# Kernel optimization log

Hardware: AMD Instinct MI355X
Metric: run time of the kernel (lower is better)

Reference implementation:

```python
import jax, jax.numpy as jnp
import numpy as np

NEARZERO = 1e-5
# Parameter bounds in dict order: BETA, FC, K0, K1, K2, LP, PERC, UZL, TT, CFMAX, CFR, CWH
BOUNDS = np.array([[1.0, 6.0], [50.0, 1000.0], [0.05, 0.9], [0.01, 0.5],
                   [0.001, 0.2], [0.2, 1.0], [0.0, 10.0], [0.0, 100.0],
                   [-2.5, 2.5], [0.5, 10.0], [0.0, 0.1], [0.0, 0.2]],
                  dtype=np.float32)


def setup_inputs() -> dict:
    key = jax.random.key(0)
    k1, k2, k3, k4 = jax.random.split(key, 4)
    T, G, nmul = 730, 4000, 8
    prcp = jax.random.uniform(k1, (T, G), dtype=jnp.float32) * 10.0   # mm/day, >= 0
    tmean = jax.random.normal(k2, (T, G), dtype=jnp.float32) * 10.0   # deg C
    pet = jax.random.uniform(k3, (T, G), dtype=jnp.float32) * 5.0     # mm/day, >= 0
    x_hydro_model = jnp.stack([prcp, tmean, pet], axis=-1)            # [T, G, 3]
    params_raw = jax.random.uniform(k4, (1, G, 12, nmul), dtype=jnp.float32)  # in [0,1)
    return {"x_hydro_model": x_hydro_model, "params_raw": params_raw}


def _hbv_forward(x_hydro_model, params_raw):
    G = x_hydro_model.shape[1]
    nmul = params_raw.shape[-1]
    b = jnp.asarray(BOUNDS)
    # change_param_range: param * (ub - lb) + lb, static slice at static_idx=-1
    p = params_raw[-1] * (b[:, 1] - b[:, 0])[None, :, None] + b[:, 0][None, :, None]  # [G,12,nmul]
    (BETA, FC, K0, K1, K2, LP, PERCc, UZL, TT, CFMAX, CFR, CWH) = [p[:, i, :] for i in range(12)]

    Pm = x_hydro_model[:, :, 0][:, :, None]    # [T, G, 1] broadcasts over nmul
    Tm = x_hydro_model[:, :, 1][:, :, None]
    PETm = x_hydro_model[:, :, 2][:, :, None]

    init = jnp.full((G, nmul), 0.001, dtype=jnp.float32)
    carry0 = (init, init, init, init, init)  # SNOWPACK, MELTWATER, SM, SUZ, SLZ

    def step(carry, inputs):
        SNOWPACK, MELTWATER, SM, SUZ, SLZ = carry
        PRECIP, Tt, PETt = inputs  # each [G, 1]
        is_rain = (Tt >= TT).astype(jnp.float32)
        RAIN = PRECIP * is_rain
        SNOW = PRECIP * (1.0 - is_rain)
        SNOWPACK = SNOWPACK + SNOW
        melt = jnp.minimum(jnp.maximum(CFMAX * (Tt - TT), 0.0), SNOWPACK)
        MELTWATER = MELTWATER + melt
        SNOWPACK = SNOWPACK - melt
        refreezing = jnp.minimum(jnp.maximum(CFR * CFMAX * (TT - Tt), 0.0), MELTWATER)
        SNOWPACK = SNOWPACK + refreezing
        MELTWATER = MELTWATER - refreezing
        tosoil = jnp.maximum(MELTWATER - CWH * SNOWPACK, 0.0)
        MELTWATER = MELTWATER - tosoil
        soil_wetness = jnp.clip((SM / FC) ** BETA, 0.0, 1.0)
        recharge = (RAIN + tosoil) * soil_wetness
        SM = SM + RAIN + tosoil - recharge
        excess = jnp.maximum(SM - FC, 0.0)
        SM = SM - excess
        evapfactor = jnp.clip(SM / (LP * FC), 0.0, 1.0)
        ETact = jnp.minimum(SM, PETt * evapfactor)
        SM = jnp.maximum(SM - ETact, NEARZERO)
        SUZ = SUZ + recharge + excess
        PERC = jnp.minimum(SUZ, PERCc)
        SUZ = SUZ - PERC
        Q0 = K0 * jnp.maximum(SUZ - UZL, 0.0)
        SUZ = SUZ - Q0
        Q1 = K1 * SUZ
        SUZ = SUZ - Q1
        SLZ = SLZ + PERC
        Q2 = K2 * SLZ
        SLZ = SLZ - Q2
        return (SNOWPACK, MELTWATER, SM, SUZ, SLZ), Q0 + Q1 + Q2

    _, Qsimmu = jax.lax.scan(step, carry0, (Pm, Tm, PETm))  # [T, G, nmul]
    return Qsimmu


def reference(x_hydro_model, params_raw):
    return _hbv_forward(x_hydro_model, params_raw)
```

## Files before the change

### kernel.cpp

```cpp
#include <hip/hip_runtime.h>
#include <math.h>
#include <stdint.h>

#define NM 8
#define NPAR 12
#define KS 32
#define NLL 3

typedef __attribute__((address_space(1))) const void gv_t;
typedef __attribute__((address_space(3))) void lv_t;
typedef float v2f __attribute__((ext_vector_type(2)));

__global__ __launch_bounds__(128, 1) void hbv_kernel(
    const float* __restrict__ x,
    const float* __restrict__ praw,
    float* __restrict__ out,
    int G, int T)
{
    __shared__ float  fbuf[2][(KS + 2) * 24];
    __shared__ float2 ring[2][KS + 2][64];

    const int wid  = threadIdx.x >> 6;
    const int lane = threadIdx.x & 63;
    const int b    = blockIdx.x;
    const int g0   = b << 3;
    const int gl   = lane >> 3;
    const int m    = lane & 7;
    const int g    = g0 + gl;

    const float lb[NPAR] = {1.0f, 50.0f, 0.05f, 0.01f, 0.001f, 0.2f, 0.0f, 0.0f, -2.5f, 0.5f, 0.0f, 0.0f};
    const float ub[NPAR] = {6.0f, 1000.0f, 0.9f, 0.5f, 0.2f, 1.0f, 10.0f, 100.0f, 2.5f, 10.0f, 0.1f, 0.2f};

    float p[NPAR];
    const float* pr = praw + (size_t)g * (NPAR * NM) + m;
    #pragma unroll
    for (int i = 0; i < NPAR; ++i) p[i] = pr[i * NM] * (ub[i] - lb[i]) + lb[i];

    const int NBLK = (T + KS - 1) / KS;

    #define ISSUE_F(fa_, pt_, e_)                                              \
        asm volatile("ds_read2_b32 %0, %2 offset0:0 offset1:1\n\t"             \
                     "ds_read_b32 %1, %2 offset:8"                             \
                     : "=v"(pt_), "=v"(e_) : "v"(fa_));
    #define WAIT_F(pt_, e_, P_, T_, E_)                                        \
        asm volatile("s_waitcnt lgkmcnt(2)\n\t"                                \
                     "v_mov_b32 %0, %3\n\t"                                    \
                     "v_mov_b32 %1, %4\n\t"                                    \
                     "v_mov_b32 %2, %5"                                        \
                     : "=v"(P_), "=v"(T_), "=v"(E_)                            \
                     : "v"(pt_.x), "v"(pt_.y), "v"(e_));
    #define ISSUE_C(ca_, rel_)                                                 \
        asm volatile("ds_read_b64 %0, %1" : "=v"(rel_) : "v"(ca_));
    #define WAIT_C(rel_, rt_, E_)                                              \
        asm volatile("s_waitcnt lgkmcnt(1)\n\t"                                \
                     "v_mov_b32 %0, %2\n\t"                                    \
                     "v_mov_b32 %1, %3"                                        \
                     : "=v"(rt_), "=v"(E_) : "v"(rel_.x), "v"(rel_.y));

    if (wid == 0) {
        const float TT = p[8], CFMAX = p[9], CFR = p[10], CWH = p[11];
        const float nCFMAX_TT   = -(CFMAX * TT);
        const float nCFRCFMAX   = -(CFR * CFMAX);
        const float CFRCFMAX_TT = (CFR * CFMAX) * TT;

        float SP = 0.001f, MW = 0.001f;

        const char* xb = (const char*)x;
        const uint32_t xstep  = (uint32_t)G * 12u;
        const uint32_t gbase  = (uint32_t)g0 * 12u;
        const uint32_t lin    = (uint32_t)lane * 16u;
        const uint32_t r0     = lin / 96u;
        const uint32_t c0     = lin % 96u;
        const uint32_t rowmax = (uint32_t)(T - 1);

        #define ISSUE_CHUNK(cs_, nb_)                                          \
        {                                                                      \
            uint32_t row_ = (uint32_t)(cs_) + r0;                              \
            uint32_t col_ = c0;                                                \
            _Pragma("unroll")                                                  \
            for (int i_ = 0; i_ < NLL; ++i_) {                                 \
                const uint32_t rg_ = row_ < rowmax ? row_ : rowmax;            \
                const uint32_t go_ = rg_ * xstep + gbase + col_;               \
                __builtin_amdgcn_global_load_lds((gv_t*)(xb + go_),            \
                    (lv_t*)&fbuf[nb_][i_ * 256], 16, 0, 0);                    \
                         \
                row_ += 10u + (col_ >= 32u ? 1u : 0u);                         \
                col_  = (col_ >= 32u) ? (col_ - 32u) : (col_ + 64u);           \
            }                                                                  \
        }

        ISSUE_CHUNK(0, 0)

        for (int r = 0; r <= NBLK; ++r) {
            if (r < NBLK) {
                if (r + 1 < NBLK) {
                    ISSUE_CHUNK((r + 1) * KS, (r + 1) & 1)
                    asm volatile("s_waitcnt vmcnt(3)" ::: "memory");
                } else {
                    asm volatile("s_waitcnt vmcnt(0)" ::: "memory");
                }
                const int cnt = (T - r * KS < KS) ? (T - r * KS) : KS;
                uint32_t fa = (uint32_t)(uintptr_t)&fbuf[r & 1][gl * 3];
                float2*  R  = &ring[r & 1][0][lane];

                v2f pt0, pt1; float e0, e1;
                ISSUE_F(fa, pt0, e0) fa += 96;
                ISSUE_F(fa, pt1, e1) fa += 96;

                #define PROD_STEP(PT_, E_)                                     \
                {                                                              \
                    float P, Tt, E;                                            \
                    WAIT_F(PT_, E_, P, Tt, E)                                  \
                    ISSUE_F(fa, PT_, E_) fa += 96;    \
                    const float RAIN = (Tt >= TT) ? P : 0.0f;                  \
                    const float SNOW = P - RAIN;                               \
                    const float mc = fmaxf(fmaf(CFMAX, Tt, nCFMAX_TT), 0.0f);  \
                    const float rc = fmaxf(fmaf(nCFRCFMAX, Tt, CFRCFMAX_TT), 0.0f); \
                    SP += SNOW;                                                \
                    const float melt = fminf(mc, SP);                          \
                    MW += melt;                                                \
                    SP -= melt;                                                \
                    const float refr = fminf(rc, MW);                          \
                    SP += refr;                                                \
                    MW -= refr;                                                \
                    const float cw = CWH * SP;                                 \
                    const float ts = fmaxf(MW - cw, 0.0f);                     \
                    MW = fminf(MW, cw);                                        \
                    float2 rel; rel.x = RAIN + ts; rel.y = E;                  \
                    *R = rel;                                                  \
                    R += 64;                                                   \
                }

                for (int tt = 0; tt < cnt; tt += 2) {
                    PROD_STEP(pt0, e0)
                    PROD_STEP(pt1, e1)
                }
                #undef PROD_STEP
            }
            __syncthreads();
        }
        #undef ISSUE_CHUNK
    } else {
        const float BETA = p[0], FC = p[1], K0 = p[2], K1 = p[3], K2 = p[4],
                    LP = p[5], PERCc = p[6], UZL = p[7];
        const float invLPFC = 1.0f / (LP * FC);
        const float nBLFC   = -BETA * __builtin_amdgcn_logf(FC);
        const float OMK0    = 1.0f - K0;
        const float K0UZL   = K0 * UZL;
        const float OMK1    = 1.0f - K1;
        const float OMK2    = 1.0f - K2;

        float SM = 0.001f, SUZ = 0.001f, SLZ = 0.001f;

        char* ob = (char*)out;
        uint32_t ooff = (uint32_t)(g * NM + m) * 4u;
        const uint32_t ostep = (uint32_t)(G * NM) * 4u;

        for (int r = 0; r <= NBLK; ++r) {
            if (r >= 1) {
                const int base = (r - 1) * KS;
                const int cnt  = (T - base < KS) ? (T - base) : KS;
                uint32_t ca = (uint32_t)(uintptr_t)&ring[(r - 1) & 1][0][lane];

                v2f rel0, rel1;
                ISSUE_C(ca, rel0) ca += 512;
                ISSUE_C(ca, rel1) ca += 512;

                #define CONS_STEP(REL_)                                        \
                {                                                              \
                    float rt, E;                                               \
                    WAIT_C(REL_, rt, E)                                        \
                    ISSUE_C(ca, REL_) ca += 512;      \
                    const float lg = __builtin_amdgcn_logf(SM);                \
                    const float bl = fminf(fmaf(BETA, lg, nBLFC), 0.0f);       \
                    const float sw = __builtin_amdgcn_exp2f(bl);               \
                    const float rg = rt * sw;                                  \
                    const float SM1 = SM + rt - rg;                            \
                    const float ex = fmaxf(SM1 - FC, 0.0f);                    \
                    const float SM2 = fminf(SM1, FC);                          \
                    const float omPe = fmaf(-E, invLPFC, 1.0f);                \
                    SM = fmaxf(fmaxf(SM2 * omPe, SM2 - E), 1e-5f);   \
                    SUZ = SUZ + rg + ex;                                       \
                    const float pc = fminf(SUZ, PERCc);                        \
                    const float s2 = fmaxf(SUZ - PERCc, 0.0f);                 \
                    const float s3 = fminf(s2, fmaf(OMK0, s2, K0UZL));         \
                    const float s4 = s3 * OMK1;                                \
                    SUZ = s4;                                                  \
                    const float sl = SLZ + pc;                                 \
                    const float q2 = K2 * sl;                                  \
                    SLZ = sl * OMK2;                                           \
                    const float Q = (s2 - s4) + q2;                            \
                    *(float*)(ob + ooff) = Q;                                  \
                    ooff += ostep;                                             \
                }

                for (int tt = 0; tt < cnt; tt += 2) {
                    CONS_STEP(rel0)
                    CONS_STEP(rel1)
                }
                #undef CONS_STEP
            }
            __syncthreads();
        }
    }
    #undef ISSUE_F
    #undef WAIT_F
    #undef ISSUE_C
    #undef WAIT_C
}

extern "C" void kernel_launch(void* const* d_in, const int* in_sizes, int n_in,
                              void* d_out, int out_size, void* d_ws, size_t ws_size,
                              hipStream_t stream) {
    const float* x    = (const float*)d_in[0];
    const float* praw = (const float*)d_in[1];
    float* out = (float*)d_out;

    const int G = in_sizes[1] / (NPAR * NM);
    const int T = in_sizes[0] / (3 * G);

    const int grid = G / 8;
    hbv_kernel<<<grid, 128, 0, stream>>>(x, praw, out, G, T);
}
```

Measured before the change: 70.88 us.

## Process two nmul members per lane and 16 gauges per block

Each lane now advances two independent HBV state chains (two nmul members) instead of one, so one block covers 16 gauges and the grid is halved. The forcing tile row width and the ring entries grow to 128-bit writes and reads, and outputs are stored as float2. The time chunk size drops from 32 to 16. The aim is to add instruction-level parallelism to the serial recurrence and to amortise LDS traffic, at the cost of half as many blocks (250 for G=4000), which lowers occupancy across the CUs.

Result: slower. 104.8 us (+47.8%).

```diff
diff --git a/kernel.cpp b/kernel.cpp
--- a/kernel.cpp
+++ b/kernel.cpp
@@ -4,12 +4,15 @@
 
 #define NM 8
 #define NPAR 12
-#define KS 32
+#define GPB 16
+#define KS 16
+#define ROWDW (GPB*3)
 #define NLL 3
 
 typedef __attribute__((address_space(1))) const void gv_t;
 typedef __attribute__((address_space(3))) void lv_t;
 typedef float v2f __attribute__((ext_vector_type(2)));
+typedef float v4f __attribute__((ext_vector_type(4)));
 
 __global__ __launch_bounds__(128, 1) void hbv_kernel(
     const float* __restrict__ x,
@@ -17,24 +20,27 @@
     float* __restrict__ out,
     int G, int T)
 {
-    __shared__ float  fbuf[2][(KS + 2) * 24];
-    __shared__ float2 ring[2][KS + 2][64];
+    __shared__ float fbuf[2][(KS + 2) * ROWDW];
+    __shared__ v4f   ring[2][KS + 2][64];
 
     const int wid  = threadIdx.x >> 6;
     const int lane = threadIdx.x & 63;
     const int b    = blockIdx.x;
-    const int g0   = b << 3;
-    const int gl   = lane >> 3;
-    const int m    = lane & 7;
-    const int g    = g0 + gl;
+    const int gl   = lane >> 2;
+    const int m0   = (lane & 3) << 1;
+    const int g    = (b << 4) + gl;
 
     const float lb[NPAR] = {1.0f, 50.0f, 0.05f, 0.01f, 0.001f, 0.2f, 0.0f, 0.0f, -2.5f, 0.5f, 0.0f, 0.0f};
     const float ub[NPAR] = {6.0f, 1000.0f, 0.9f, 0.5f, 0.2f, 1.0f, 10.0f, 100.0f, 2.5f, 10.0f, 0.1f, 0.2f};
 
-    float p[NPAR];
-    const float* pr = praw + (size_t)g * (NPAR * NM) + m;
+    float pA[NPAR], pB[NPAR];
+    const float* pr = praw + (size_t)g * (NPAR * NM) + m0;
     #pragma unroll
-    for (int i = 0; i < NPAR; ++i) p[i] = pr[i * NM] * (ub[i] - lb[i]) + lb[i];
+    for (int i = 0; i < NPAR; ++i) {
+        const float s = ub[i] - lb[i];
+        pA[i] = pr[i * NM]     * s + lb[i];
+        pB[i] = pr[i * NM + 1] * s + lb[i];
+    }
 
     const int NBLK = (T + KS - 1) / KS;
 
@@ -47,30 +53,37 @@
                      "v_mov_b32 %0, %3\n\t"                                    \
                      "v_mov_b32 %1, %4\n\t"                                    \
                      "v_mov_b32 %2, %5"                                        \
-                     : "=v"(P_), "=v"(T_), "=v"(E_)                            \
+                     : "=&v"(P_), "=&v"(T_), "=&v"(E_)                         \
                      : "v"(pt_.x), "v"(pt_.y), "v"(e_));
+    #define WRITE_R(wa_, w_)                                                   \
+        asm volatile("ds_write_b128 %0, %1" :: "v"(wa_), "v"(w_));
     #define ISSUE_C(ca_, rel_)                                                 \
-        asm volatile("ds_read_b64 %0, %1" : "=v"(rel_) : "v"(ca_));
-    #define WAIT_C(rel_, rt_, E_)                                              \
+        asm volatile("ds_read_b128 %0, %1" : "=v"(rel_) : "v"(ca_));
+    #define WAIT_C(rel_, rtA_, EA_, rtB_, EB_)                                 \
         asm volatile("s_waitcnt lgkmcnt(1)\n\t"                                \
-                     "v_mov_b32 %0, %2\n\t"                                    \
-                     "v_mov_b32 %1, %3"                                        \
-                     : "=v"(rt_), "=v"(E_) : "v"(rel_.x), "v"(rel_.y));
+                     "v_mov_b32 %0, %4\n\t"                                    \
+                     "v_mov_b32 %1, %5\n\t"                                    \
+                     "v_mov_b32 %2, %6\n\t"                                    \
+                     "v_mov_b32 %3, %7"                                        \
+                     : "=&v"(rtA_), "=&v"(EA_), "=&v"(rtB_), "=&v"(EB_)        \
+                     : "v"(rel_.x), "v"(rel_.y), "v"(rel_.z), "v"(rel_.w));
 
     if (wid == 0) {
-        const float TT = p[8], CFMAX = p[9], CFR = p[10], CWH = p[11];
-        const float nCFMAX_TT   = -(CFMAX * TT);
-        const float nCFRCFMAX   = -(CFR * CFMAX);
-        const float CFRCFMAX_TT = (CFR * CFMAX) * TT;
-
-        float SP = 0.001f, MW = 0.001f;
+        const float TTa = pA[8],  TTb = pB[8];
+        const float CFa = pA[9],  CFb = pB[9];
+        const float nCMa = -(CFa * TTa),          nCMb = -(CFb * TTb);
+        const float nCRa = -(pA[10] * CFa),       nCRb = -(pB[10] * CFb);
+        const float CRTa = (pA[10] * CFa) * TTa,  CRTb = (pB[10] * CFb) * TTb;
+        const float CWa  = pA[11],                CWb  = pB[11];
+
+        float SPa = 0.001f, MWa = 0.001f, SPb = 0.001f, MWb = 0.001f;
 
         const char* xb = (const char*)x;
         const uint32_t xstep  = (uint32_t)G * 12u;
-        const uint32_t gbase  = (uint32_t)g0 * 12u;
+        const uint32_t gbase  = (uint32_t)(b << 4) * 12u;
         const uint32_t lin    = (uint32_t)lane * 16u;
-        const uint32_t r0     = lin / 96u;
-        const uint32_t c0     = lin % 96u;
+        const uint32_t r0     = lin / 192u;
+        const uint32_t c0     = lin % 192u;
         const uint32_t rowmax = (uint32_t)(T - 1);
 
         #define ISSUE_CHUNK(cs_, nb_)                                          \
@@ -84,8 +97,8 @@
                 __builtin_amdgcn_global_load_lds((gv_t*)(xb + go_),            \
                     (lv_t*)&fbuf[nb_][i_ * 256], 16, 0, 0);                    \
                          \
-                row_ += 10u + (col_ >= 32u ? 1u : 0u);                         \
-                col_  = (col_ >= 32u) ? (col_ - 32u) : (col_ + 64u);           \
+                row_ += 5u + (col_ >= 128u ? 1u : 0u);                         \
+                col_  = (col_ >= 128u) ? (col_ - 128u) : (col_ + 64u);         \
             }                                                                  \
         }
 
@@ -101,59 +114,69 @@
                 }
                 const int cnt = (T - r * KS < KS) ? (T - r * KS) : KS;
                 uint32_t fa = (uint32_t)(uintptr_t)&fbuf[r & 1][gl * 3];
-                float2*  R  = &ring[r & 1][0][lane];
+                uint32_t wa = (uint32_t)(uintptr_t)&ring[r & 1][0][lane];
 
                 v2f pt0, pt1; float e0, e1;
-                ISSUE_F(fa, pt0, e0) fa += 96;
-                ISSUE_F(fa, pt1, e1) fa += 96;
-
-                #define PROD_STEP(PT_, E_)                                     \
+                v4f w0, w1;
+                ISSUE_F(fa, pt0, e0) fa += 192;
+                ISSUE_F(fa, pt1, e1) fa += 192;
+
+                #define PROD_STEP(PT_, E_, W_)                                 \
                 {                                                              \
                     float P, Tt, E;                                            \
                     WAIT_F(PT_, E_, P, Tt, E)                                  \
-                    ISSUE_F(fa, PT_, E_) fa += 96;    \
-                    const float RAIN = (Tt >= TT) ? P : 0.0f;                  \
-                    const float SNOW = P - RAIN;                               \
-                    const float mc = fmaxf(fmaf(CFMAX, Tt, nCFMAX_TT), 0.0f);  \
-                    const float rc = fmaxf(fmaf(nCFRCFMAX, Tt, CFRCFMAX_TT), 0.0f); \
-                    SP += SNOW;                                                \
-                    const float melt = fminf(mc, SP);                          \
-                    MW += melt;                                                \
-                    SP -= melt;                                                \
-                    const float refr = fminf(rc, MW);                          \
-                    SP += refr;                                                \
-                    MW -= refr;                                                \
-                    const float cw = CWH * SP;                                 \
-                    const float ts = fmaxf(MW - cw, 0.0f);                     \
-                    MW = fminf(MW, cw);                                        \
-                    float2 rel; rel.x = RAIN + ts; rel.y = E;                  \
-                    *R = rel;                                                  \
-                    R += 64;                                                   \
+                    const float rnA = (Tt >= TTa) ? P : 0.0f;                  \
+                    const float rnB = (Tt >= TTb) ? P : 0.0f;                  \
+                    const float mcA = fmaxf(fmaf(CFa, Tt, nCMa), 0.0f);        \
+                    const float mcB = fmaxf(fmaf(CFb, Tt, nCMb), 0.0f);        \
+                    const float rcA = fmaxf(fmaf(nCRa, Tt, CRTa), 0.0f);       \
+                    const float rcB = fmaxf(fmaf(nCRb, Tt, CRTb), 0.0f);       \
+                    SPa += P - rnA;                 SPb += P - rnB;            \
+                    const float mA = fminf(mcA, SPa);                          \
+                    const float mB = fminf(mcB, SPb);                          \
+                    MWa += mA; SPa -= mA;           MWb += mB; SPb -= mB;      \
+                    const float rA = fminf(rcA, MWa);                          \
+                    const float rB = fminf(rcB, MWb);                          \
+                    SPa += rA; MWa -= rA;           SPb += rB; MWb -= rB;      \
+                    const float cA = CWa * SPa;     const float cB = CWb * SPb;\
+                    const float tA = fmaxf(MWa - cA, 0.0f);                    \
+                    const float tB = fmaxf(MWb - cB, 0.0f);                    \
+                    MWa = fminf(MWa, cA);           MWb = fminf(MWb, cB);      \
+                    W_.x = rnA + tA; W_.y = E; W_.z = rnB + tB; W_.w = E;      \
+                    WRITE_R(wa, W_)                                            \
+                    wa += 1024;                                                \
+                    ISSUE_F(fa, PT_, E_)              \
+                    fa += 192;                                                 \
                 }
 
                 for (int tt = 0; tt < cnt; tt += 2) {
-                    PROD_STEP(pt0, e0)
-                    PROD_STEP(pt1, e1)
+                    PROD_STEP(pt0, e0, w0)
+                    PROD_STEP(pt1, e1, w1)
                 }
                 #undef PROD_STEP
             }
+            asm volatile("s_waitcnt lgkmcnt(0)" ::: "memory");
             __syncthreads();
         }
         #undef ISSUE_CHUNK
     } else {
-        const float BETA = p[0], FC = p[1], K0 = p[2], K1 = p[3], K2 = p[4],
-                    LP = p[5], PERCc = p[6], UZL = p[7];
-        const float invLPFC = 1.0f / (LP * FC);
-        const float nBLFC   = -BETA * __builtin_amdgcn_logf(FC);
-        const float OMK0    = 1.0f - K0;
-        const float K0UZL   = K0 * UZL;
-        const float OMK1    = 1.0f - K1;
-        const float OMK2    = 1.0f - K2;
-
-        float SM = 0.001f, SUZ = 0.001f, SLZ = 0.001f;
+        const float BEa = pA[0], BEb = pB[0];
+        const float FCa = pA[1], FCb = pB[1];
+        const float iLa = 1.0f / (pA[5] * FCa),  iLb = 1.0f / (pB[5] * FCb);
+        const float nBa = -BEa * __builtin_amdgcn_logf(FCa);
+        const float nBb = -BEb * __builtin_amdgcn_logf(FCb);
+        const float OK0a = 1.0f - pA[2],  OK0b = 1.0f - pB[2];
+        const float KUa  = pA[2] * pA[7], KUb  = pB[2] * pB[7];
+        const float OK1a = 1.0f - pA[3],  OK1b = 1.0f - pB[3];
+        const float PCa  = pA[6],         PCb  = pB[6];
+        const float K2a  = pA[4],         K2b  = pB[4];
+        const float OK2a = 1.0f - K2a,    OK2b = 1.0f - K2b;
+
+        float SMa = 0.001f, SUa = 0.001f, SLa = 0.001f;
+        float SMb = 0.001f, SUb = 0.001f, SLb = 0.001f;
 
         char* ob = (char*)out;
-        uint32_t ooff = (uint32_t)(g * NM + m) * 4u;
+        uint32_t ooff = (uint32_t)((b << 7) + (lane << 1)) * 4u;
         const uint32_t ostep = (uint32_t)(G * NM) * 4u;
 
         for (int r = 0; r <= NBLK; ++r) {
@@ -162,35 +185,48 @@
                 const int cnt  = (T - base < KS) ? (T - base) : KS;
                 uint32_t ca = (uint32_t)(uintptr_t)&ring[(r - 1) & 1][0][lane];
 
-                v2f rel0, rel1;
-                ISSUE_C(ca, rel0) ca += 512;
-                ISSUE_C(ca, rel1) ca += 512;
+                v4f rel0, rel1;
+                ISSUE_C(ca, rel0) ca += 1024;
+                ISSUE_C(ca, rel1) ca += 1024;
 
                 #define CONS_STEP(REL_)                                        \
                 {                                                              \
-                    float rt, E;                                               \
-                    WAIT_C(REL_, rt, E)                                        \
-                    ISSUE_C(ca, REL_) ca += 512;      \
-                    const float lg = __builtin_amdgcn_logf(SM);                \
-                    const float bl = fminf(fmaf(BETA, lg, nBLFC), 0.0f);       \
-                    const float sw = __builtin_amdgcn_exp2f(bl);               \
-                    const float rg = rt * sw;                                  \
-                    const float SM1 = SM + rt - rg;                            \
-                    const float ex = fmaxf(SM1 - FC, 0.0f);                    \
-                    const float SM2 = fminf(SM1, FC);                          \
-                    const float omPe = fmaf(-E, invLPFC, 1.0f);                \
-                    SM = fmaxf(fmaxf(SM2 * omPe, SM2 - E), 1e-5f);   \
-                    SUZ = SUZ + rg + ex;                                       \
-                    const float pc = fminf(SUZ, PERCc);                        \
-                    const float s2 = fmaxf(SUZ - PERCc, 0.0f);                 \
-                    const float s3 = fminf(s2, fmaf(OMK0, s2, K0UZL));         \
-                    const float s4 = s3 * OMK1;                                \
-                    SUZ = s4;                                                  \
-                    const float sl = SLZ + pc;                                 \
-                    const float q2 = K2 * sl;                                  \
-                    SLZ = sl * OMK2;                                           \
-                    const float Q = (s2 - s4) + q2;                            \
-                    *(float*)(ob + ooff) = Q;                                  \
+                    float rtA, EA, rtB, EB;                                    \
+                    WAIT_C(REL_, rtA, EA, rtB, EB)                             \
+                    ISSUE_C(ca, REL_) ca += 1024;     \
+                                                     \
+                    const float lgA = __builtin_amdgcn_logf(SMa);              \
+                    const float lgB = __builtin_amdgcn_logf(SMb);              \
+                    const float blA = fminf(fmaf(BEa, lgA, nBa), 0.0f);        \
+                    const float blB = fminf(fmaf(BEb, lgB, nBb), 0.0f);        \
+                    const float swA = __builtin_amdgcn_exp2f(blA);             \
+                    const float swB = __builtin_amdgcn_exp2f(blB);             \
+                    const float rgA = rtA * swA;     const float rgB = rtB * swB; \
+                    const float S1A = SMa + rtA - rgA;                         \
+                    const float S1B = SMb + rtB - rgB;                         \
+                    const float exA = fmaxf(S1A - FCa, 0.0f);                  \
+                    const float exB = fmaxf(S1B - FCb, 0.0f);                  \
+                    const float S2A = fminf(S1A, FCa);                         \
+                    const float S2B = fminf(S1B, FCb);                         \
+                    const float oPA = fmaf(-EA, iLa, 1.0f);                    \
+                    const float oPB = fmaf(-EB, iLb, 1.0f);                    \
+                    SMa = fmaxf(fmaxf(S2A * oPA, S2A - EA), 1e-5f);            \
+                    SMb = fmaxf(fmaxf(S2B * oPB, S2B - EB), 1e-5f);            \
+                                          \
+                    SUa = SUa + rgA + exA;           SUb = SUb + rgB + exB;    \
+                    const float pcA = fminf(SUa, PCa);                         \
+                    const float pcB = fminf(SUb, PCb);                         \
+                    const float s2A = fmaxf(SUa - PCa, 0.0f);                  \
+                    const float s2B = fmaxf(SUb - PCb, 0.0f);                  \
+                    const float s3A = fminf(s2A, fmaf(OK0a, s2A, KUa));        \
+                    const float s3B = fminf(s2B, fmaf(OK0b, s2B, KUb));        \
+                    const float s4A = s3A * OK1a;    const float s4B = s3B * OK1b; \
+                    SUa = s4A;                       SUb = s4B;                \
+                    const float slA = SLa + pcA;     const float slB = SLb + pcB; \
+                    const float q2A = K2a * slA;     const float q2B = K2b * slB; \
+                    SLa = slA * OK2a;                SLb = slB * OK2b;         \
+                    v2f q; q.x = (s2A - s4A) + q2A;  q.y = (s2B - s4B) + q2B;  \
+                    *(v2f*)(ob + ooff) = q;            \
                     ooff += ostep;                                             \
                 }
 
@@ -205,6 +241,7 @@
     }
     #undef ISSUE_F
     #undef WAIT_F
+    #undef WRITE_R
     #undef ISSUE_C
     #undef WAIT_C
 }
@@ -219,6 +256,6 @@
     const int G = in_sizes[1] / (NPAR * NM);
     const int T = in_sizes[0] / (3 * G);
 
-    const int grid = G / 8;
+    const int grid = G / GPB;
     hbv_kernel<<<grid, 128, 0, stream>>>(x, praw, out, G, T);
 }
```
